# Optimization experiments

Hardware: AMD Instinct MI355X
Metric: run time of the kernel (lower is better)

The kernel has to match this reference:

```python
import jax, jax.numpy as jnp
import numpy as np
import math

B, S, E = 16, 600, 300   # batch, seq_len, enc_len
H, NC = 512, 2           # hidden, classes
D = S * E                # archi[0] = 180000


def setup_inputs() -> dict:
    key = jax.random.key(0)
    ks = jax.random.split(key, 7)
    x = jax.random.normal(ks[0], (B, S, E), dtype=jnp.float32)
    y = jax.random.randint(ks[1], (B,), 0, NC)
    # neurons initialized to zeros (init_neurons)
    n0 = jnp.zeros((B, S, E), jnp.float32)
    n1 = jnp.zeros((B, H), jnp.float32)
    n2 = jnp.zeros((B, NC), jnp.float32)
    # Linear weights (torch layout: [out, in]), Kaiming-uniform-like scale 1/sqrt(fan_in)
    W0 = jax.random.uniform(ks[2], (E, E), jnp.float32, -1.0, 1.0) / math.sqrt(E)
    W1 = jax.random.uniform(ks[3], (H, D), jnp.float32, -1.0, 1.0) / math.sqrt(D)
    b1 = jax.random.uniform(ks[4], (H,), jnp.float32, -1.0, 1.0) / math.sqrt(D)
    W2 = jax.random.uniform(ks[5], (NC, H), jnp.float32, -1.0, 1.0) / math.sqrt(H)
    b2 = jax.random.uniform(ks[6], (NC,), jnp.float32, -1.0, 1.0) / math.sqrt(H)
    return dict(x=x, y=y, n0=n0, n1=n1, n2=n2, W0=W0, W1=W1, b1=b1, W2=W2, b2=b2, T=3)


def reference(x, y, n0, n1, n2, W0, W1, b1, W2, b2, T):
    # EqProp free-phase relaxation (beta = 0.0, forward default).
    # Analytic dPhi/dneurons replaces torch.autograd.grad:
    scale = 1.0 / math.sqrt(E)
    Wx = jnp.einsum('bse,fe->bsf', x, W0)  # synapses[0](x), constant across steps
    for _ in range(T):
        g0 = Wx + (n1 @ W1).reshape(B, S, E)              # dPhi/dn0
        g1 = n0.reshape(B, D) @ W1.T + b1 + n2 @ W2       # dPhi/dn1
        g2 = n1 @ W2.T + b2                               # dPhi/dn2 (beta=0)
        # hand-coded attention update for neuron 0: Q=g0, K=V=x
        attn = jax.nn.softmax(scale * jnp.einsum('bse,bte->bst', g0, x), axis=-1)
        n0 = jnp.einsum('bst,bte->bse', attn, x)
        n1 = jnp.tanh(g1)
        n2 = jnp.tanh(g2)
    return n0, n1, n2
```

## Files before the change

### kernel.cpp

```cpp
#include <hip/hip_runtime.h>
#include <math.h>

#define DD 180000L
#define HH 512
#define BB 16
#define SS 600
#define EE 300
#define SP 608
#define EP 320

typedef unsigned short u16;
typedef __attribute__((ext_vector_type(8))) __bf16 bf16x8;
typedef __attribute__((ext_vector_type(4))) float f32x4;

__device__ __forceinline__ u16 f2bf(float f) {
  union { float f; unsigned int u; } x; x.f = f;
  unsigned int r = (x.u + 0x7FFFu + ((x.u >> 16) & 1u)) >> 16;
  return (u16)r;
}

__global__ __launch_bounds__(256) void k_conv_x(const float* __restrict__ x,
                                                u16* __restrict__ xb, u16* __restrict__ xt) {
  __shared__ u16 tl[32][33];
  int b = blockIdx.z;
  int tt = blockIdx.x * 32, ee = blockIdx.y * 32;
  int lx = threadIdx.x & 31, ly = threadIdx.x >> 5;
#pragma unroll
  for (int i = 0; i < 4; ++i) {
    int t = tt + ly + i * 8, e = ee + lx;
    float v = (t < SS && e < EE) ? x[((long)b * SS + t) * EE + e] : 0.f;
    u16 h = f2bf(v);
    xb[((long)b * SP + t) * EP + e] = h;
    tl[ly + i * 8][lx] = h;
  }
  __syncthreads();
#pragma unroll
  for (int i = 0; i < 4; ++i) {
    int e = ee + ly + i * 8, t = tt + lx;
    xt[((long)b * EP + e) * SP + t] = tl[lx][ly + i * 8];
  }
}

__global__ __launch_bounds__(256) void k_conv_w0(const float* __restrict__ W0, u16* __restrict__ w0b) {
  int idx = blockIdx.x * 256 + threadIdx.x;
  int f = idx / EP, e = idx % EP;
  float v = (f < EE && e < EE) ? W0[f * EE + e] : 0.f;
  w0b[idx] = f2bf(v);
}

__global__ __launch_bounds__(256) void k_gemm_nt(
    const u16* __restrict__ A, int lda, long sA, int Arows,
    const u16* __restrict__ B, int ldb, long sB, int Brows,
    float* __restrict__ C, int ldc, long sC, int Mv, int Nv, int K,
    u16* __restrict__ Cb, int ldcb, long sCb) {
  int bz = blockIdx.z;
  int m0 = blockIdx.x * 64, n0 = blockIdx.y * 64;
  int lane = threadIdx.x & 63, wv = threadIdx.x >> 6;
  int wm = m0 + (wv >> 1) * 32, wn = n0 + (wv & 1) * 32;
  int q = lane >> 4, ln = lane & 15;
  const u16* Ab = A + (long)bz * sA;
  const u16* Bb = B + (long)bz * sB;
  long arow0 = (long)min(wm + ln, Arows - 1) * lda;
  long arow1 = (long)min(wm + 16 + ln, Arows - 1) * lda;
  long brow0 = (long)min(wn + ln, Brows - 1) * ldb;
  long brow1 = (long)min(wn + 16 + ln, Brows - 1) * ldb;
  f32x4 acc00 = {0.f,0.f,0.f,0.f}, acc01 = acc00, acc10 = acc00, acc11 = acc00;
  int ksteps = (K + 31) >> 5;
  for (int kk = 0; kk < ksteps; ++kk) {
    int k0 = kk * 32 + q * 8;
    bf16x8 a0 = *(const bf16x8*)(Ab + arow0 + k0);
    bf16x8 a1 = *(const bf16x8*)(Ab + arow1 + k0);
    bf16x8 b0 = *(const bf16x8*)(Bb + brow0 + k0);
    bf16x8 bv1 = *(const bf16x8*)(Bb + brow1 + k0);
    acc00 = __builtin_amdgcn_mfma_f32_16x16x32_bf16(a0, b0,  acc00, 0, 0, 0);
    acc01 = __builtin_amdgcn_mfma_f32_16x16x32_bf16(a0, bv1, acc01, 0, 0, 0);
    acc10 = __builtin_amdgcn_mfma_f32_16x16x32_bf16(a1, b0,  acc10, 0, 0, 0);
    acc11 = __builtin_amdgcn_mfma_f32_16x16x32_bf16(a1, bv1, acc11, 0, 0, 0);
  }
  float* Cp = C + (long)bz * sC;
  u16* Cbp = Cb ? (Cb + (long)bz * sCb) : (u16*)0;
#pragma unroll
  for (int sm = 0; sm < 2; ++sm) {
#pragma unroll
    for (int sn = 0; sn < 2; ++sn) {
      f32x4 acc = (sm == 0) ? ((sn == 0) ? acc00 : acc01) : ((sn == 0) ? acc10 : acc11);
#pragma unroll
      for (int r = 0; r < 4; ++r) {
        int m = wm + sm * 16 + q * 4 + r;
        int n = wn + sn * 16 + ln;
        if (m < Mv && n < Nv) {
          float v = acc[r];
          Cp[(long)m * ldc + n] = v;
          if (Cbp) Cbp[(long)m * ldcb + n] = f2bf(v);
        }
      }
    }
  }
}

#define BN 256
#define BK 64
#define NCH 704

__global__ __launch_bounds__(256) void k_fused_w1(
    const float* __restrict__ W1, const float* __restrict__ n1f,
    const float* __restrict__ n0f, const float* __restrict__ Wx,
    u16* __restrict__ g0b, float* __restrict__ part) {
  __shared__ u16 wt[BK][BN + 8];
  __shared__ u16 n1s[BB][HH + 8];
  __shared__ u16 n0s[BB][BN + 8];
  int tid = threadIdx.x;
  long d0 = (long)blockIdx.x * BN;
#pragma unroll
  for (int i = 0; i < 8; ++i) {
    int f = i * 256 + tid;
    int b = f >> 7, c = (f & 127) * 4;
    float4 v = *(const float4*)(n1f + b * HH + c);
    n1s[b][c] = f2bf(v.x); n1s[b][c + 1] = f2bf(v.y);
    n1s[b][c + 2] = f2bf(v.z); n1s[b][c + 3] = f2bf(v.w);
  }
#pragma unroll
  for (int i = 0; i < 4; ++i) {
    int f = i * 256 + tid;
    int b = f >> 6, c = (f & 63) * 4;
    long d = d0 + c;
    float4 v = {0.f,0.f,0.f,0.f};
    if (d < DD) v = *(const float4*)(n0f + (long)b * DD + d);
    n0s[b][c] = f2bf(v.x); n0s[b][c + 1] = f2bf(v.y);
    n0s[b][c + 2] = f2bf(v.z); n0s[b][c + 3] = f2bf(v.w);
  }
  int lane = tid & 63, wv = tid >> 6, q = lane >> 4, ln = lane & 15;
  f32x4 acc0[4] = {{0.f,0.f,0.f,0.f},{0.f,0.f,0.f,0.f},{0.f,0.f,0.f,0.f},{0.f,0.f,0.f,0.f}};
  for (int s = 0; s < 8; ++s) {
    int h0 = s * BK;
    __syncthreads();
#pragma unroll
    for (int i = 0; i < 16; ++i) {
      int f = i * 256 + tid;
      int r = f >> 6, c = (f & 63) * 4;
      long d = d0 + c;
      float4 v = {0.f,0.f,0.f,0.f};
      if (d < DD) v = *(const float4*)(W1 + (long)(h0 + r) * DD + d);
      wt[r][c] = f2bf(v.x); wt[r][c + 1] = f2bf(v.y);
      wt[r][c + 2] = f2bf(v.z); wt[r][c + 3] = f2bf(v.w);
    }
    __syncthreads();
#pragma unroll
    for (int kst = 0; kst < 2; ++kst) {
      bf16x8 af = *(const bf16x8*)(&n1s[ln][h0 + kst * 32 + q * 8]);
#pragma unroll
      for (int nt = 0; nt < 4; ++nt) {
        int dc = wv * 64 + nt * 16 + ln;
        bf16x8 bv;
#pragma unroll
        for (int j = 0; j < 8; ++j) bv[j] = *(const __bf16*)(&wt[kst * 32 + q * 8 + j][dc]);
        acc0[nt] = __builtin_amdgcn_mfma_f32_16x16x32_bf16(af, bv, acc0[nt], 0, 0, 0);
      }
    }
    f32x4 acc1 = {0.f,0.f,0.f,0.f};
#pragma unroll
    for (int kst = 0; kst < 8; ++kst) {
      bf16x8 af = *(const bf16x8*)(&n0s[ln][kst * 32 + q * 8]);
      bf16x8 bv = *(const bf16x8*)(&wt[wv * 16 + ln][kst * 32 + q * 8]);
      acc1 = __builtin_amdgcn_mfma_f32_16x16x32_bf16(af, bv, acc1, 0, 0, 0);
    }
    long pb = (long)blockIdx.x * 8192;
#pragma unroll
    for (int r = 0; r < 4; ++r) {
      int b = q * 4 + r, h = h0 + wv * 16 + ln;
      part[pb + b * HH + h] = acc1[r];
    }
  }
#pragma unroll
  for (int nt = 0; nt < 4; ++nt) {
#pragma unroll
    for (int r = 0; r < 4; ++r) {
      int b = q * 4 + r;
      long d = d0 + wv * 64 + nt * 16 + ln;
      if (d < DD) {
        float val = Wx[(long)b * DD + d] + acc0[nt][r];
        int sI = (int)(d / EE), e = (int)(d % EE);
        g0b[((long)b * SS + sI) * EP + e] = f2bf(val);
      }
    }
  }
}

#define SWZB(r) ((((r) >> 1) & 7) << 4)

__global__ __launch_bounds__(64, 2) void k_attn(
    const u16* __restrict__ Qg, const u16* __restrict__ Kg,
    const u16* __restrict__ Vtg, float* __restrict__ O, float scale) {
  __shared__ u16 P[16 * SP];
  int b = blockIdx.y, tile = blockIdx.x;
  int lane = threadIdx.x;
  int q = lane >> 4, ln = lane & 15, q4 = q * 4;
  const u16* Qb = Qg + (long)b * SS * EP;
  const u16* Kb = Kg + (long)b * SP * EP;
  const u16* Vb = Vtg + (long)b * EP * SP;

  int qrow = min(tile * 16 + ln, SS - 1);
  bf16x8 qf[10];
#pragma unroll
  for (int kk = 0; kk < 10; ++kk)
    qf[kk] = *(const bf16x8*)(Qb + (long)qrow * EP + kk * 32 + q * 8);

  f32x4 s[38];
#pragma unroll
  for (int j = 0; j < 38; ++j) {
    const u16* Kr = Kb + (long)(j * 16 + ln) * EP + q * 8;
    f32x4 sa = {0.f, 0.f, 0.f, 0.f}, sb = {0.f, 0.f, 0.f, 0.f};
#pragma unroll
    for (int kk = 0; kk < 10; kk += 2) {
      bf16x8 k0 = *(const bf16x8*)(Kr + kk * 32);
      bf16x8 k1 = *(const bf16x8*)(Kr + kk * 32 + 32);
      sa = __builtin_amdgcn_mfma_f32_16x16x32_bf16(qf[kk], k0, sa, 0, 0, 0);
      sb = __builtin_amdgcn_mfma_f32_16x16x32_bf16(qf[kk + 1], k1, sb, 0, 0, 0);
    }
    s[j] = sa + sb;
  }

  float mx[4] = {-3e38f, -3e38f, -3e38f, -3e38f};
#pragma unroll
  for (int j = 0; j < 38; ++j) {
    bool msk = (j == 37) && (ln >= 8);
#pragma unroll
    for (int r = 0; r < 4; ++r) {
      float v = msk ? -3e38f : s[j][r];
      mx[r] = fmaxf(mx[r], v);
    }
  }
#pragma unroll
  for (int off = 8; off; off >>= 1)
#pragma unroll
    for (int r = 0; r < 4; ++r) mx[r] = fmaxf(mx[r], __shfl_xor(mx[r], off));
  float sm[4] = {0.f, 0.f, 0.f, 0.f};
#pragma unroll
  for (int j = 0; j < 38; ++j) {
    bool msk = (j == 37) && (ln >= 8);
#pragma unroll
    for (int r = 0; r < 4; ++r) {
      float e = msk ? 0.f : __expf(scale * (s[j][r] - mx[r]));
      s[j][r] = e;
      sm[r] += e;
    }
  }
#pragma unroll
  for (int off = 8; off; off >>= 1)
#pragma unroll
    for (int r = 0; r < 4; ++r) sm[r] += __shfl_xor(sm[r], off);
#pragma unroll
  for (int r = 0; r < 4; ++r) sm[r] = 1.f / sm[r];

#pragma unroll
  for (int j = 0; j < 38; ++j) {
#pragma unroll
    for (int r = 0; r < 4; ++r) {
      int row = q4 + r, t = j * 16 + ln;
      unsigned byt = (unsigned)row * 1216 + (unsigned)t * 2;
      P[(byt ^ SWZB(row)) >> 1] = f2bf(s[j][r] * sm[r]);
    }
  }

  f32x4 acc[19];
#pragma unroll
  for (int nt = 0; nt < 19; ++nt) acc[nt] = (f32x4){0.f, 0.f, 0.f, 0.f};
#pragma unroll
  for (int kt = 0; kt < 19; ++kt) {
    unsigned byt = (unsigned)ln * 1216 + (unsigned)kt * 64 + (unsigned)q * 16;
    bf16x8 pa = *(const bf16x8*)(&P[(byt ^ SWZB(ln)) >> 1]);
#pragma unroll
    for (int nt = 0; nt < 19; ++nt) {
      bf16x8 bv = *(const bf16x8*)(Vb + (long)(nt * 16 + ln) * SP + kt * 32 + q * 8);
      acc[nt] = __builtin_amdgcn_mfma_f32_16x16x32_bf16(pa, bv, acc[nt], 0, 0, 0);
    }
  }

  float* Ob = O + (long)b * SS * EE;
  int m0 = tile * 16 + q4;
#pragma unroll
  for (int nt = 0; nt < 19; ++nt) {
#pragma unroll
    for (int r = 0; r < 4; ++r) {
      int m = m0 + r, n = nt * 16 + ln;
      if (m < SS && n < EE) Ob[(long)m * EE + n] = acc[nt][r];
    }
  }
}

__global__ __launch_bounds__(256) void k_init(const float* __restrict__ b1, const float* __restrict__ b2,
                                              float* __restrict__ n1, float* __restrict__ n2) {
  int idx = blockIdx.x * 256 + threadIdx.x;
  n1[idx] = tanhf(b1[idx & 511]);
  if (idx < 32) n2[idx] = tanhf(b2[idx & 1]);
}

__global__ __launch_bounds__(64) void k_g2(const float* __restrict__ n1old, const float* __restrict__ W2,
                                           const float* __restrict__ b2, float* __restrict__ n2out) {
  int b = blockIdx.x >> 1, c = blockIdx.x & 1, lane = threadIdx.x;
  float s = 0.f;
#pragma unroll
  for (int i = 0; i < 8; ++i) { int h = lane + i * 64; s += n1old[b * HH + h] * W2[c * HH + h]; }
  for (int off = 32; off; off >>= 1) s += __shfl_down(s, off);
  if (lane == 0) n2out[b * 2 + c] = tanhf(s + b2[c]);
}

__global__ __launch_bounds__(256) void k_reduce1(const float* __restrict__ part, float* __restrict__ part2) {
  int idx = blockIdx.x * 256 + threadIdx.x;
  int sl = blockIdx.y;
  float s = 0.f;
  int c0 = sl * 88;
#pragma unroll 4
  for (int c = 0; c < 88; ++c) s += part[(long)(c0 + c) * 8192 + idx];
  part2[(long)sl * 8192 + idx] = s;
}

__global__ __launch_bounds__(256) void k_reduce2(const float* __restrict__ part2, const float* __restrict__ b1,
                                                 const float* __restrict__ W2, const float* __restrict__ n2old,
                                                 float* __restrict__ n1out) {
  int idx = blockIdx.x * 256 + threadIdx.x;
  int b = idx >> 9, h = idx & 511;
  float s = b1[h] + n2old[b * 2] * W2[h] + n2old[b * 2 + 1] * W2[HH + h];
#pragma unroll
  for (int sl = 0; sl < 8; ++sl) s += part2[(long)sl * 8192 + idx];
  n1out[idx] = tanhf(s);
}

extern "C" void kernel_launch(void* const* d_in, const int* in_sizes, int n_in,
                              void* d_out, int out_size, void* d_ws, size_t ws_size,
                              hipStream_t stream) {
  const float* x  = (const float*)d_in[0];
  const float* W0 = (const float*)d_in[5];
  const float* W1 = (const float*)d_in[6];
  const float* b1 = (const float*)d_in[7];
  const float* W2 = (const float*)d_in[8];
  const float* b2 = (const float*)d_in[9];

  float* out_n0 = (float*)d_out;
  float* out_n1 = out_n0 + 16L * SS * EE;
  float* out_n2 = out_n1 + 16L * HH;

  char* w = (char*)d_ws;
  auto take = [&](size_t bytes) { char* p = w; w += (bytes + 255) & ~(size_t)255; return p; };
  u16*   xb    = (u16*)take(16L * SP * EP * 2);
  u16*   xt    = (u16*)take(16L * EP * SP * 2);
  u16*   w0b   = (u16*)take((size_t)EP * EP * 2);
  float* Wx    = (float*)take(16L * SS * EE * 4);
  u16*   g0b   = (u16*)take(16L * SS * EP * 2);
  float* part  = (float*)take((size_t)NCH * 8192 * 4);
  float* part2 = (float*)take(8L * 8192 * 4);
  float* n1A   = (float*)take(8192 * 4);
  float* n1B   = (float*)take(8192 * 4);
  float* n2A   = (float*)take(256);
  float* n2B   = (float*)take(256);

  const float scale = 1.0f / sqrtf((float)EE);

  k_conv_x<<<dim3(19, 10, 16), 256, 0, stream>>>(x, xb, xt);
  k_conv_w0<<<400, 256, 0, stream>>>(W0, w0b);
  k_gemm_nt<<<dim3(10, 5, 16), 256, 0, stream>>>(xb, EP, (long)SP * EP, SP,
                                                 w0b, EP, 0, EP,
                                                 Wx, EE, (long)SS * EE, SS, EE, EE,
                                                 g0b, EP, (long)SS * EP);
  k_init<<<32, 256, 0, stream>>>(b1, b2, n1A, n2A);

  for (int it = 0; it < 3; ++it) {
    if (it > 0) {
      const float* n1old = (it == 1) ? n1A : n1B;
      const float* n2old = (it == 1) ? n2A : n2B;
      float* n2new = (it == 1) ? n2B : out_n2;
      float* n1new = (it == 1) ? n1B : out_n1;
      k_g2<<<32, 64, 0, stream>>>(n1old, W2, b2, n2new);
      k_fused_w1<<<NCH, 256, 0, stream>>>(W1, n1old, out_n0, Wx, g0b, part);
      k_reduce1<<<dim3(32, 8), 256, 0, stream>>>(part, part2);
      k_reduce2<<<32, 256, 0, stream>>>(part2, b1, W2, n2old, n1new);
    }
    k_attn<<<dim3(38, 16), 64, 0, stream>>>(g0b, xb, xt, out_n0, scale);
  }
}
```

Measured before the change: 1.065 ms.

## Split attention tile across four waves with cross-wave softmax reduction

The attention kernel now uses four wavefronts per 16-row query tile instead of one. Each wave computes a strided subset of key tiles and output column tiles, and the softmax max and sum are combined across waves through shared memory. This cuts per-thread register pressure (s[38] becomes s[10], acc[19] becomes acc[5]) and adds parallelism per tile. Block indices are also remapped so that neighbouring blocks spread across XCDs, at the cost of extra barriers and redundant Q loads in every wave.

```diff
diff --git a/kernel.cpp b/kernel.cpp
--- a/kernel.cpp
+++ b/kernel.cpp
@@ -188,12 +188,16 @@
 
 #define SWZB(r) ((((r) >> 1) & 7) << 4)
 
-__global__ __launch_bounds__(64, 2) void k_attn(
+__global__ __launch_bounds__(256, 2) void k_attn(
     const u16* __restrict__ Qg, const u16* __restrict__ Kg,
     const u16* __restrict__ Vtg, float* __restrict__ O, float scale) {
   __shared__ u16 P[16 * SP];
-  int b = blockIdx.y, tile = blockIdx.x;
-  int lane = threadIdx.x;
+  __shared__ float red[2][4][16];
+  int orig = blockIdx.x + blockIdx.y * gridDim.x;
+  int wg = (orig & 7) * 76 + (orig >> 3);
+  int tile = wg % 38, b = wg / 38;
+  int tid = threadIdx.x;
+  int w = tid >> 6, lane = tid & 63;
   int q = lane >> 4, ln = lane & 15, q4 = q * 4;
   const u16* Qb = Qg + (long)b * SS * EP;
   const u16* Kb = Kg + (long)b * SP * EP;
@@ -205,85 +209,117 @@
   for (int kk = 0; kk < 10; ++kk)
     qf[kk] = *(const bf16x8*)(Qb + (long)qrow * EP + kk * 32 + q * 8);
 
-  f32x4 s[38];
-#pragma unroll
-  for (int j = 0; j < 38; ++j) {
-    const u16* Kr = Kb + (long)(j * 16 + ln) * EP + q * 8;
+  f32x4 s[10];
+#pragma unroll
+  for (int i = 0; i < 10; ++i) {
+    int j = w + 4 * i;
     f32x4 sa = {0.f, 0.f, 0.f, 0.f}, sb = {0.f, 0.f, 0.f, 0.f};
-#pragma unroll
-    for (int kk = 0; kk < 10; kk += 2) {
-      bf16x8 k0 = *(const bf16x8*)(Kr + kk * 32);
-      bf16x8 k1 = *(const bf16x8*)(Kr + kk * 32 + 32);
-      sa = __builtin_amdgcn_mfma_f32_16x16x32_bf16(qf[kk], k0, sa, 0, 0, 0);
-      sb = __builtin_amdgcn_mfma_f32_16x16x32_bf16(qf[kk + 1], k1, sb, 0, 0, 0);
-    }
-    s[j] = sa + sb;
+    if (j < 38) {
+      const u16* Kr = Kb + (long)(j * 16 + ln) * EP + q * 8;
+#pragma unroll
+      for (int kk = 0; kk < 10; kk += 2) {
+        bf16x8 k0 = *(const bf16x8*)(Kr + kk * 32);
+        bf16x8 k1 = *(const bf16x8*)(Kr + kk * 32 + 32);
+        sa = __builtin_amdgcn_mfma_f32_16x16x32_bf16(qf[kk], k0, sa, 0, 0, 0);
+        sb = __builtin_amdgcn_mfma_f32_16x16x32_bf16(qf[kk + 1], k1, sb, 0, 0, 0);
+      }
+    }
+    s[i] = sa + sb;
   }
 
   float mx[4] = {-3e38f, -3e38f, -3e38f, -3e38f};
 #pragma unroll
-  for (int j = 0; j < 38; ++j) {
-    bool msk = (j == 37) && (ln >= 8);
-#pragma unroll
-    for (int r = 0; r < 4; ++r) {
-      float v = msk ? -3e38f : s[j][r];
-      mx[r] = fmaxf(mx[r], v);
+  for (int i = 0; i < 10; ++i) {
+    int j = w + 4 * i;
+    if (j < 38) {
+      bool msk = (j == 37) && (ln >= 8);
+#pragma unroll
+      for (int r = 0; r < 4; ++r) mx[r] = fmaxf(mx[r], msk ? -3e38f : s[i][r]);
     }
   }
 #pragma unroll
   for (int off = 8; off; off >>= 1)
 #pragma unroll
     for (int r = 0; r < 4; ++r) mx[r] = fmaxf(mx[r], __shfl_xor(mx[r], off));
+  if (ln == 0) {
+#pragma unroll
+    for (int r = 0; r < 4; ++r) red[0][w][q4 + r] = mx[r];
+  }
+  __syncthreads();
+#pragma unroll
+  for (int r = 0; r < 4; ++r)
+    mx[r] = fmaxf(fmaxf(red[0][0][q4 + r], red[0][1][q4 + r]),
+                  fmaxf(red[0][2][q4 + r], red[0][3][q4 + r]));
   float sm[4] = {0.f, 0.f, 0.f, 0.f};
 #pragma unroll
-  for (int j = 0; j < 38; ++j) {
-    bool msk = (j == 37) && (ln >= 8);
-#pragma unroll
-    for (int r = 0; r < 4; ++r) {
-      float e = msk ? 0.f : __expf(scale * (s[j][r] - mx[r]));
-      s[j][r] = e;
-      sm[r] += e;
+  for (int i = 0; i < 10; ++i) {
+    int j = w + 4 * i;
+    if (j < 38) {
+      bool msk = (j == 37) && (ln >= 8);
+#pragma unroll
+      for (int r = 0; r < 4; ++r) {
+        float e = msk ? 0.f : __expf(scale * (s[i][r] - mx[r]));
+        s[i][r] = e;
+        sm[r] += e;
+      }
     }
   }
 #pragma unroll
   for (int off = 8; off; off >>= 1)
 #pragma unroll
     for (int r = 0; r < 4; ++r) sm[r] += __shfl_xor(sm[r], off);
-#pragma unroll
-  for (int r = 0; r < 4; ++r) sm[r] = 1.f / sm[r];
-
-#pragma unroll
-  for (int j = 0; j < 38; ++j) {
-#pragma unroll
-    for (int r = 0; r < 4; ++r) {
-      int row = q4 + r, t = j * 16 + ln;
-      unsigned byt = (unsigned)row * 1216 + (unsigned)t * 2;
-      P[(byt ^ SWZB(row)) >> 1] = f2bf(s[j][r] * sm[r]);
-    }
-  }
-
-  f32x4 acc[19];
-#pragma unroll
-  for (int nt = 0; nt < 19; ++nt) acc[nt] = (f32x4){0.f, 0.f, 0.f, 0.f};
+  if (ln == 0) {
+#pragma unroll
+    for (int r = 0; r < 4; ++r) red[1][w][q4 + r] = sm[r];
+  }
+  __syncthreads();
+#pragma unroll
+  for (int r = 0; r < 4; ++r)
+    sm[r] = 1.f / (red[1][0][q4 + r] + red[1][1][q4 + r] +
+                   red[1][2][q4 + r] + red[1][3][q4 + r]);
+
+#pragma unroll
+  for (int i = 0; i < 10; ++i) {
+    int j = w + 4 * i;
+    if (j < 38) {
+#pragma unroll
+      for (int r = 0; r < 4; ++r) {
+        int row = q4 + r, t = j * 16 + ln;
+        unsigned byt = (unsigned)row * 1216 + (unsigned)t * 2;
+        P[(byt ^ SWZB(row)) >> 1] = f2bf(s[i][r] * sm[r]);
+      }
+    }
+  }
+  __syncthreads();
+
+  f32x4 acc[5];
+#pragma unroll
+  for (int i = 0; i < 5; ++i) acc[i] = (f32x4){0.f, 0.f, 0.f, 0.f};
 #pragma unroll
   for (int kt = 0; kt < 19; ++kt) {
     unsigned byt = (unsigned)ln * 1216 + (unsigned)kt * 64 + (unsigned)q * 16;
     bf16x8 pa = *(const bf16x8*)(&P[(byt ^ SWZB(ln)) >> 1]);
 #pragma unroll
-    for (int nt = 0; nt < 19; ++nt) {
-      bf16x8 bv = *(const bf16x8*)(Vb + (long)(nt * 16 + ln) * SP + kt * 32 + q * 8);
-      acc[nt] = __builtin_amdgcn_mfma_f32_16x16x32_bf16(pa, bv, acc[nt], 0, 0, 0);
+    for (int i = 0; i < 5; ++i) {
+      int nt = w + 4 * i;
+      if (nt < 19) {
+        bf16x8 bv = *(const bf16x8*)(Vb + (long)(nt * 16 + ln) * SP + kt * 32 + q * 8);
+        acc[i] = __builtin_amdgcn_mfma_f32_16x16x32_bf16(pa, bv, acc[i], 0, 0, 0);
+      }
     }
   }
 
   float* Ob = O + (long)b * SS * EE;
   int m0 = tile * 16 + q4;
 #pragma unroll
-  for (int nt = 0; nt < 19; ++nt) {
-#pragma unroll
-    for (int r = 0; r < 4; ++r) {
-      int m = m0 + r, n = nt * 16 + ln;
-      if (m < SS && n < EE) Ob[(long)m * EE + n] = acc[nt][r];
+  for (int i = 0; i < 5; ++i) {
+    int nt = w + 4 * i;
+    if (nt < 19) {
+#pragma unroll
+      for (int r = 0; r < 4; ++r) {
+        int m = m0 + r, n = nt * 16 + ln;
+        if (m < SS && n < EE) Ob[(long)m * EE + n] = acc[i][r];
+      }
     }
   }
 }
@@ -375,6 +411,6 @@
       k_reduce1<<<dim3(32, 8), 256, 0, stream>>>(part, part2);
       k_reduce2<<<32, 256, 0, stream>>>(part2, b1, W2, n2old, n1new);
     }
-    k_attn<<<dim3(38, 16), 64, 0, stream>>>(g0b, xb, xt, out_n0, scale);
-  }
-}
+    k_attn<<<dim3(38, 16), 256, 0, stream>>>(g0b, xb, xt, out_n0, scale);
+  }
+}
```

New measurement: 959.6 us. 9.9% less time.
